# Kernel tuning notes

Measured on AMD Instinct MI355X. Metric: run time of the kernel, lower is better.

Reference implementation:

```python
import jax, jax.numpy as jnp
import numpy as np

IN_SIZE = 1024
OUT_SIZE = 3 * IN_SIZE  # must equal 3*in_size for trigger_a * attn broadcast
B, S = 32, 512


def setup_inputs() -> dict:
    key = jax.random.key(0)
    ks = jax.random.split(key, 8)
    h_state = jax.random.normal(ks[0], (B, S, 2 * IN_SIZE), dtype=jnp.float32)
    x = jax.random.normal(ks[1], (B, S, IN_SIZE), dtype=jnp.float32)
    trigger = jax.random.randint(ks[2], (B,), 0, S)
    mask = jax.random.randint(ks[3], (B, S), 0, 2).astype(jnp.int32)
    # learned params (nn.Linear: y = x @ W.T + b; store pre-transposed as (in, out))
    Wa = jax.random.normal(ks[4], (3 * IN_SIZE, OUT_SIZE), dtype=jnp.float32) / np.sqrt(3 * IN_SIZE)
    ba = jnp.zeros((OUT_SIZE,), dtype=jnp.float32)
    Ws = jax.random.normal(ks[5], (2 * IN_SIZE, OUT_SIZE), dtype=jnp.float32) / np.sqrt(2 * IN_SIZE)
    bs = jnp.zeros((OUT_SIZE,), dtype=jnp.float32)
    return {"h_state": h_state, "x": x, "trigger": trigger, "mask": mask,
            "Wa": Wa, "ba": ba, "Ws": Ws, "bs": bs}


def reference(h_state, x, trigger, mask, Wa, ba, Ws, bs):
    # a: (B, S, 3*in_size)
    a = jnp.concatenate([h_state, x], axis=-1)
    b = a.shape[0]
    # one_hot + masked_select in the original == gather of the trigger row per batch
    trigger_a = a[jnp.arange(b), trigger]  # (B, 3*in_size)
    s = h_state.sum(axis=1)  # (B, 2*in_size)
    # et: (B, S, out_size)
    et = jnp.tanh(a @ Wa + ba + (s @ Ws + bs)[:, None, :])
    # masked_fill where mask == 0 (mask broadcast over feature dim)
    et = jnp.where(mask[:, :, None] == 0, jnp.float32(-1e9), et)
    # softmax over the FEATURE dim (dim=-1), as in the original; dropout in eval mode is identity
    attn = jax.nn.softmax(et, axis=-1)
    # trigger-weighted reduction over the sequence dim
    out = (trigger_a[:, None, :] * attn).sum(axis=1)  # (B, out_size)
    return out
```

## Files before the change

### kernel.cpp

```cpp
#include <hip/hip_runtime.h>
#include <hip/hip_bf16.h>
#include <hip/hip_fp16.h>


namespace {
constexpr int SIN  = 1024;
constexpr int KH   = 2048;
constexpr int NF   = 3072;
constexpr int NBAT = 32;
constexpr int NS   = 512;
constexpr int NM   = NBAT * NS;
constexpr int NDB  = NF / 64;
constexpr int KC   = 8;
constexpr int NKT  = NF / 64;
constexpr int NCH  = 8;
}

typedef unsigned short u16;
typedef __bf16 bf16x8 __attribute__((ext_vector_type(8)));
typedef float  f32x4  __attribute__((ext_vector_type(4)));

#define ASYNC_CP16(gptr, lptr)                                                              \
  __builtin_amdgcn_global_load_lds((__attribute__((address_space(1))) void*)(gptr),         \
                                   (__attribute__((address_space(3))) void*)(lptr), 16, 0, 0)

__device__ __forceinline__ u16 f2b(float f) {
  union { float f; unsigned u; } v; v.f = f;
  unsigned u = v.u;
  u += 0x7FFFu + ((u >> 16) & 1u);
  return (u16)(u >> 16);
}

__global__ __launch_bounds__(64) void k_cnt(const int* __restrict__ mask,
                                            int* __restrict__ bcnt) {
  int b = blockIdx.x, t = threadIdx.x;
  int c = 0;
#pragma unroll
  for (int i = 0; i < NS / 64; ++i) c += mask[b * NS + i * 64 + t];
#pragma unroll
  for (int off = 32; off >= 1; off >>= 1) c += __shfl_down(c, off, 64);
  if (t == 0) bcnt[b] = c;
}

__global__ __launch_bounds__(64) void k_scan(const int* __restrict__ bcnt,
                                             int* __restrict__ boff,
                                             int* __restrict__ meta) {
  if (threadIdx.x == 0) {
    int run = 0;
    for (int b = 0; b < NBAT; ++b) { boff[b] = run; run += bcnt[b]; }
    meta[0] = run;
    meta[1] = (run + 255) & ~255;
  }
}

__global__ __launch_bounds__(512) void k_gather(const int* __restrict__ mask,
                                                const int* __restrict__ boff,
                                                const int* __restrict__ meta,
                                                int* __restrict__ rowmap) {
  __shared__ int ps[NS];
  int b = blockIdx.x, t = threadIdx.x;
  int m = mask[b * NS + t];
  ps[t] = m;
  __syncthreads();
#pragma unroll
  for (int off = 1; off < NS; off <<= 1) {
    int v = (t >= off) ? ps[t - off] : 0;
    __syncthreads();
    ps[t] += v;
    __syncthreads();
  }
  if (m) rowmap[boff[b] + ps[t] - m] = b * NS + t;
  if (b == 0) {
    int Mc = meta[0], McPad = meta[1];
    if (Mc + t < McPad) rowmap[Mc + t] = 0;
  }
}

__global__ __launch_bounds__(256) void k_sum_h(const float* __restrict__ h,
                                               float* __restrict__ s) {
  int b = blockIdx.x;
  int d = blockIdx.y * 256 + threadIdx.x;
  const float* p = h + (size_t)b * NS * KH + d;
  float acc = 0.f;
#pragma unroll 8
  for (int t = 0; t < NS; ++t) acc += p[(size_t)t * KH];
  s[b * KH + d] = acc;
}

__global__ __launch_bounds__(256) void k_base1(const float* __restrict__ s,
                                               const float* __restrict__ Ws,
                                               float* __restrict__ basep) {
  __shared__ float sT[NBAT][KH / KC];
  int f  = blockIdx.x * 256 + threadIdx.x;
  int k0 = blockIdx.y * (KH / KC);
  for (int it = 0; it < NBAT; ++it) {
    int idx = it * 256 + threadIdx.x;
    int b = idx >> 8, kk = idx & 255;
    sT[b][kk] = s[b * KH + k0 + kk];
  }
  __syncthreads();
  float acc[NBAT] = {};
  for (int k = 0; k < KH / KC; ++k) {
    float w = Ws[(size_t)(k0 + k) * NF + f];
#pragma unroll
    for (int b = 0; b < NBAT; ++b) acc[b] += sT[b][k] * w;
  }
#pragma unroll
  for (int b = 0; b < NBAT; ++b)
    basep[((size_t)blockIdx.y * NBAT + b) * NF + f] = acc[b];
}

__global__ __launch_bounds__(256) void k_base2(const float* __restrict__ basep,
                                               const float* __restrict__ ba,
                                               const float* __restrict__ bs,
                                               float* __restrict__ base) {
  int b = blockIdx.x;
  int f = blockIdx.y * 256 + threadIdx.x;
  float acc = 0.f;
#pragma unroll
  for (int kc = 0; kc < KC; ++kc) acc += basep[((size_t)kc * NBAT + b) * NF + f];
  base[b * NF + f] = acc + ba[f] + bs[f];
}

__global__ __launch_bounds__(256) void k_cvt_a(const float* __restrict__ h,
                                               const float* __restrict__ x,
                                               const int* __restrict__ rowmap,
                                               const int* __restrict__ meta,
                                               u16* __restrict__ A) {
  int tid = blockIdx.x * 256 + threadIdx.x;
  int i = tid / (NF / 4);
  if (i >= meta[1]) return;
  int k = (tid - i * (NF / 4)) * 4;
  ushort4 o;
  if (i >= meta[0]) {
    o.x = o.y = o.z = o.w = 0;
  } else {
    int ro = rowmap[i];
    int b = ro >> 9, t = ro & 511;
    const float* src = (k < KH) ? h + ((size_t)b * NS + t) * KH + k
                                : x + ((size_t)b * NS + t) * SIN + (k - KH);
    float4 v = *(const float4*)src;
    o.x = f2b(v.x); o.y = f2b(v.y); o.z = f2b(v.z); o.w = f2b(v.w);
  }
  *(ushort4*)(A + (size_t)i * NF + k) = o;
}

__global__ __launch_bounds__(256) void k_wat(const float* __restrict__ Wa,
                                             u16* __restrict__ WaT) {
  __shared__ float tile[64][65];
  int k0 = blockIdx.x * 64, f0 = blockIdx.y * 64;
  int tid = threadIdx.x;
  int col4 = (tid & 15) * 4, row = tid >> 4;
#pragma unroll
  for (int rr = 0; rr < 64; rr += 16) {
    float4 v = *(const float4*)(Wa + (size_t)(k0 + row + rr) * NF + f0 + col4);
    tile[row + rr][col4 + 0] = v.x; tile[row + rr][col4 + 1] = v.y;
    tile[row + rr][col4 + 2] = v.z; tile[row + rr][col4 + 3] = v.w;
  }
  __syncthreads();
#pragma unroll
  for (int rr = 0; rr < 64; rr += 16) {
    int f = f0 + row + rr;
    ushort4 o;
    o.x = f2b(tile[col4 + 0][row + rr]); o.y = f2b(tile[col4 + 1][row + rr]);
    o.z = f2b(tile[col4 + 2][row + rr]); o.w = f2b(tile[col4 + 3][row + rr]);
    *(ushort4*)(WaT + (size_t)f * NF + k0 + col4) = o;
  }
}

#define LDSOFF(row, gg) ((row) * 32 + ((((gg) ^ (((row) >> 1) & 3))) << 3))

#define LDB4(BUF, KS)                                                        \
  _Pragma("unroll") for (int nf = 0; nf < 4; ++nf) {                         \
    int rb = wc * 64 + nf * 16 + lr;                                         \
    bfr[nf] = *(const bf16x8*)&lds[BUF][1][KS][LDSOFF(rb, g)];               \
  }

#define LDA4(BUF, KS, MH)                                                    \
  _Pragma("unroll") for (int mf = 0; mf < 4; ++mf) {                         \
    int ra = wr * 128 + ((MH) * 4 + mf) * 16 + lr;                           \
    afr[mf] = *(const bf16x8*)&lds[BUF][0][KS][LDSOFF(ra, g)];               \
  }

#define MFMA16(MH)                                                           \
  _Pragma("unroll") for (int mf = 0; mf < 4; ++mf)                           \
  _Pragma("unroll") for (int nf = 0; nf < 4; ++nf)                           \
    acc[(MH) * 4 + mf][nf] = __builtin_amdgcn_mfma_f32_16x16x32_bf16(        \
        afr[mf], bfr[nf], acc[(MH) * 4 + mf][nf], 0, 0, 0);

#define STAGE(SMAT, SBUF, SKS, SKT)                                          \
  if ((SKT) < NKT) {                                                         \
    _Pragma("unroll") for (int q = 0; q < 2; ++q) {                          \
      const u16* src = ((SMAT) ? pB[q] : pA[q]) + (SKT) * 64 + (SKS) * 32;   \
      ASYNC_CP16(src, &lds[SBUF][SMAT][SKS][q * 4096 + wid * 512]);          \
    }                                                                        \
  }

#define PH(BUF, KS, MH, SMAT, SBUF, SKS, SKT)                                \
  {                                                                          \
    if ((MH) == 0) { LDB4(BUF, KS) }                                         \
    LDA4(BUF, KS, MH)                                                        \
    STAGE(SMAT, SBUF, SKS, SKT)                                              \
    __builtin_amdgcn_s_barrier();                                            \
    asm volatile("s_waitcnt lgkmcnt(0)" ::: "memory");                       \
    __builtin_amdgcn_s_setprio(1);                                           \
    MFMA16(MH)                                                               \
    __builtin_amdgcn_s_setprio(0);                                           \
    asm volatile("s_waitcnt vmcnt(6)" ::: "memory");                         \
    __builtin_amdgcn_s_barrier();                                            \
  }

__global__ __launch_bounds__(512, 2) void k_gemm(const u16* __restrict__ A,
                                                 const u16* __restrict__ Wt,
                                                 const float* __restrict__ base,
                                                 const int* __restrict__ rowmap,
                                                 const int* __restrict__ meta,
                                                 __half* __restrict__ P,
                                                 float* __restrict__ Dpart) {
  __shared__ __align__(16) u16 lds[2][2][2][8192];
  const int MT   = meta[1] >> 8;
  const int nact = MT * 12;
  const int flat = blockIdx.x;
  if (flat >= nact) return;
  const int qx = nact >> 3, rx = nact & 7;
  const int xcd = flat & 7, idx = flat >> 3;
  const int swz = (xcd < rx) ? xcd * (qx + 1) + idx
                             : rx * (qx + 1) + (xcd - rx) * qx + idx;
  const int mt = swz / 12, nt = swz - mt * 12;
  const int r0 = mt << 8, c0 = nt << 8;

  const int tid = threadIdx.x;
  const int wid = tid >> 6, lane = tid & 63;
  const int wr = wid >> 2, wc = wid & 3;
  const int g = lane >> 4, lr = lane & 15;

  const u16* pA[2]; const u16* pB[2];
#pragma unroll
  for (int q = 0; q < 2; ++q) {
    int c = q * 512 + tid;
    int row = c >> 2;
    int kc8 = (((c & 3) ^ ((row >> 1) & 3)) << 3);
    pA[q] = A  + (size_t)(r0 + row) * NF + kc8;
    pB[q] = Wt + (size_t)(c0 + row) * NF + kc8;
  }

  f32x4 acc[8][4] = {};
  bf16x8 afr[4], bfr[4];

  STAGE(0, 0, 0, 0) STAGE(1, 0, 0, 0)
  STAGE(0, 0, 1, 0) STAGE(1, 0, 1, 0)
  STAGE(0, 1, 0, 1) STAGE(1, 1, 0, 1)
  asm volatile("s_waitcnt vmcnt(8)" ::: "memory");
  __builtin_amdgcn_s_barrier();

#pragma unroll 1
  for (int i = 0; i < NKT / 2; ++i) {
    const int kt1 = 2 * i + 1, kt2 = 2 * i + 2, kt3 = 2 * i + 3;
    PH(0, 0, 0, 0, 1, 1, kt1)
    PH(0, 0, 1, 1, 1, 1, kt1)
    PH(0, 1, 0, 0, 0, 0, kt2)
    PH(0, 1, 1, 1, 0, 0, kt2)
    PH(1, 0, 0, 0, 0, 1, kt2)
    PH(1, 0, 1, 1, 0, 1, kt2)
    PH(1, 1, 0, 0, 1, 0, kt3)
    PH(1, 1, 1, 1, 1, 0, kt3)
  }

  const int cbase = c0 + wc * 64;
#pragma unroll
  for (int mf = 0; mf < 8; ++mf) {
#pragma unroll
    for (int j = 0; j < 4; ++j) {
      int i = r0 + wr * 128 + mf * 16 + g * 4 + j;
      int b = rowmap[i] >> 9;
      float rs = 0.f;
#pragma unroll
      for (int nf = 0; nf < 4; ++nf) {
        int ccn = cbase + nf * 16 + lr;
        float z  = acc[mf][nf][j] + base[b * NF + ccn];
        z        = fminf(fmaxf(z, -15.f), 15.f);
        float e2 = __expf(2.f * z);
        float th = (e2 - 1.f) / (e2 + 1.f);
        float p  = __expf(th);
        P[(size_t)i * NF + ccn] = __float2half(p);
        rs += p;
      }
#pragma unroll
      for (int off = 1; off < 16; off <<= 1) rs += __shfl_xor(rs, off, 64);
      if (lr == 0) Dpart[(size_t)i * NDB + (cbase >> 6)] = rs;
    }
  }
}

__global__ __launch_bounds__(256) void k_invd(const float* __restrict__ Dpart,
                                              const int* __restrict__ meta,
                                              float* __restrict__ invD) {
  int i = blockIdx.x * 256 + threadIdx.x;
  if (i >= meta[1]) return;
  float d = 0.f;
#pragma unroll
  for (int q = 0; q < NDB; ++q) d += Dpart[(size_t)i * NDB + q];
  invD[i] = 1.0f / d;
}

__global__ __launch_bounds__(256) void k_final1(const __half* __restrict__ P,
                                                const float* __restrict__ invD,
                                                const int* __restrict__ boff,
                                                const int* __restrict__ bcnt,
                                                float* __restrict__ pb) {
  int c = blockIdx.x;
  int b = c >> 3, j = c & 7;
  int f = blockIdx.y * 256 + threadIdx.x;
  int cnt = bcnt[b];
  int lo = j * 64, hi = min(cnt, lo + 64);
  int off = boff[b];
  float acc = 0.f;
  for (int t = lo; t < hi; ++t)
    acc += __half2float(P[(size_t)(off + t) * NF + f]) * invD[off + t];
  pb[(size_t)c * NF + f] = acc;
}

__global__ __launch_bounds__(256) void k_final2(const float* __restrict__ pb,
                                                const int* __restrict__ bcnt,
                                                const float* __restrict__ h,
                                                const float* __restrict__ x,
                                                const int* __restrict__ trig,
                                                float* __restrict__ out) {
  int b = blockIdx.x;
  int f = blockIdx.y * 256 + threadIdx.x;
  float acc = 0.f;
#pragma unroll
  for (int j = 0; j < NCH; ++j) acc += pb[(size_t)(b * NCH + j) * NF + f];
  acc += (float)(NS - bcnt[b]) * (1.0f / (float)NF);
  int tr = trig[b];
  float ta = (f < KH) ? h[((size_t)b * NS + tr) * KH + f]
                      : x[((size_t)b * NS + tr) * SIN + f - KH];
  out[b * NF + f] = acc * ta;
}

extern "C" void kernel_launch(void* const* d_in, const int* in_sizes, int n_in,
                              void* d_out, int out_size, void* d_ws, size_t ws_size,
                              hipStream_t stream) {
  const float* h_state = (const float*)d_in[0];
  const float* x       = (const float*)d_in[1];
  const int*   trigger = (const int*)d_in[2];
  const int*   mask    = (const int*)d_in[3];
  const float* Wa      = (const float*)d_in[4];
  const float* ba      = (const float*)d_in[5];
  const float* Ws      = (const float*)d_in[6];
  const float* bs      = (const float*)d_in[7];
  float*       out     = (float*)d_out;

  char* w = (char*)d_ws;
  u16*    Abf   = (u16*)w;                 w += (size_t)NM * NF * 2;
  u16*    WaT   = (u16*)w;                 w += (size_t)NF * NF * 2;
  __half* P     = (__half*)w;              w += (size_t)NM * NF * 2;
  float*  s     = (float*)w;               w += (size_t)NBAT * KH * 4;
  float*  base  = (float*)w;               w += (size_t)NBAT * NF * 4;
  float*  Dpart = (float*)w;               w += (size_t)NM * NDB * 4;
  float*  basep = (float*)Dpart;
  float*  pb    = (float*)Dpart;
  float*  invD  = (float*)w;               w += (size_t)NM * 4;
  int*    rowmap= (int*)w;                 w += (size_t)NM * 4;
  int*    bcnt  = (int*)w;                 w += 128;
  int*    boff  = (int*)w;                 w += 128;
  int*    meta  = (int*)w;                 w += 128;

  (void)in_sizes; (void)n_in; (void)out_size; (void)ws_size;

  k_cnt   <<<dim3(NBAT), 64, 0, stream>>>(mask, bcnt);
  k_scan  <<<dim3(1), 64, 0, stream>>>(bcnt, boff, meta);
  k_gather<<<dim3(NBAT), 512, 0, stream>>>(mask, boff, meta, rowmap);
  k_sum_h <<<dim3(NBAT, KH / 256), 256, 0, stream>>>(h_state, s);
  k_cvt_a <<<dim3(NM * (NF / 4) / 256), 256, 0, stream>>>(h_state, x, rowmap, meta, Abf);
  k_wat   <<<dim3(NF / 64, NF / 64), 256, 0, stream>>>(Wa, WaT);
  k_base1 <<<dim3(NF / 256, KC), 256, 0, stream>>>(s, Ws, basep);
  k_base2 <<<dim3(NBAT, NF / 256), 256, 0, stream>>>(basep, ba, bs, base);
  k_gemm  <<<dim3((NF / 256) * (NM / 256)), 512, 0, stream>>>(Abf, WaT, base, rowmap, meta, P, Dpart);
  k_invd  <<<dim3(NM / 256), 256, 0, stream>>>(Dpart, meta, invD);
  k_final1<<<dim3(NBAT * NCH, NF / 256), 256, 0, stream>>>(P, invD, boff, bcnt, pb);
  k_final2<<<dim3(NBAT, NF / 256), 256, 0, stream>>>(pb, bcnt, h_state, x, trigger, out);
}
```

Measured before the change: 423.0 us.

## Fuse h-sum with masked bf16 row compaction; merge count/scan; vectorize final1

Merges the mask count and scan kernels into one single-block kernel. Replaces the separate sequence-sum and gather-convert kernels with one kernel that streams h once, accumulating per-chunk partial sums while writing compacted bf16 rows of A. Pad-row zeroing moves into the gather kernel, and the per-chunk partial sums are reduced inside base1. final1 now processes two features per thread with half2 loads and caches invD in shared memory. The fused kernel launches only 256 blocks, each walking 64 rows serially, which may leave much of the GPU idle.

```diff
diff --git a/kernel.cpp b/kernel.cpp
--- a/kernel.cpp
+++ b/kernel.cpp
@@ -31,23 +31,24 @@
   return (u16)(u >> 16);
 }
 
-__global__ __launch_bounds__(64) void k_cnt(const int* __restrict__ mask,
-                                            int* __restrict__ bcnt) {
-  int b = blockIdx.x, t = threadIdx.x;
+__global__ __launch_bounds__(256) void k_prep(const int* __restrict__ mask,
+                                              int* __restrict__ bcnt,
+                                              int* __restrict__ boff,
+                                              int* __restrict__ meta) {
+  int tid = threadIdx.x;
+  int b = tid >> 3, seg = tid & 7;
   int c = 0;
 #pragma unroll
-  for (int i = 0; i < NS / 64; ++i) c += mask[b * NS + i * 64 + t];
-#pragma unroll
-  for (int off = 32; off >= 1; off >>= 1) c += __shfl_down(c, off, 64);
-  if (t == 0) bcnt[b] = c;
-}
-
-__global__ __launch_bounds__(64) void k_scan(const int* __restrict__ bcnt,
-                                             int* __restrict__ boff,
-                                             int* __restrict__ meta) {
-  if (threadIdx.x == 0) {
+  for (int i = 0; i < 64; ++i) c += mask[b * NS + seg * 64 + i];
+  c += __shfl_xor(c, 1, 64);
+  c += __shfl_xor(c, 2, 64);
+  c += __shfl_xor(c, 4, 64);
+  __shared__ int sc[NBAT];
+  if (seg == 0) { sc[b] = c; bcnt[b] = c; }
+  __syncthreads();
+  if (tid == 0) {
     int run = 0;
-    for (int b = 0; b < NBAT; ++b) { boff[b] = run; run += bcnt[b]; }
+    for (int bb = 0; bb < NBAT; ++bb) { boff[bb] = run; run += sc[bb]; }
     meta[0] = run;
     meta[1] = (run + 255) & ~255;
   }
@@ -56,7 +57,8 @@
 __global__ __launch_bounds__(512) void k_gather(const int* __restrict__ mask,
                                                 const int* __restrict__ boff,
                                                 const int* __restrict__ meta,
-                                                int* __restrict__ rowmap) {
+                                                int* __restrict__ rowmap,
+                                                u16* __restrict__ A) {
   __shared__ int ps[NS];
   int b = blockIdx.x, t = threadIdx.x;
   int m = mask[b * NS + t];
@@ -70,33 +72,73 @@
     __syncthreads();
   }
   if (m) rowmap[boff[b] + ps[t] - m] = b * NS + t;
-  if (b == 0) {
-    int Mc = meta[0], McPad = meta[1];
-    if (Mc + t < McPad) rowmap[Mc + t] = 0;
-  }
-}
-
-__global__ __launch_bounds__(256) void k_sum_h(const float* __restrict__ h,
-                                               float* __restrict__ s) {
-  int b = blockIdx.x;
-  int d = blockIdx.y * 256 + threadIdx.x;
-  const float* p = h + (size_t)b * NS * KH + d;
-  float acc = 0.f;
-#pragma unroll 8
-  for (int t = 0; t < NS; ++t) acc += p[(size_t)t * KH];
-  s[b * KH + d] = acc;
-}
-
-__global__ __launch_bounds__(256) void k_base1(const float* __restrict__ s,
+  int Mc = meta[0], pad = meta[1] - Mc;
+  if (b == 0 && t < 256) { if (t < pad) rowmap[Mc + t] = 0; }
+  for (int r = b; r < pad; r += NBAT) {
+    unsigned* row = (unsigned*)(A + (size_t)(Mc + r) * NF);
+    for (int u = t; u < NF / 2; u += 512) row[u] = 0;
+  }
+}
+
+__global__ __launch_bounds__(256) void k_pre(const float* __restrict__ h,
+                                             const float* __restrict__ x,
+                                             const int* __restrict__ mask,
+                                             const int* __restrict__ boff,
+                                             float* __restrict__ spart,
+                                             u16* __restrict__ A) {
+  int b = blockIdx.x, tc = blockIdx.y, tid = threadIdx.x;
+  __shared__ int red[256];
+  __shared__ int ms[64];
+  int pre = 0;
+  for (int u = tid; u < tc * 64; u += 256) pre += mask[b * NS + u];
+  red[tid] = pre;
+  if (tid < 64) ms[tid] = mask[b * NS + tc * 64 + tid];
+  __syncthreads();
+#pragma unroll
+  for (int s2 = 128; s2 > 0; s2 >>= 1) {
+    if (tid < s2) red[tid] += red[tid + s2];
+    __syncthreads();
+  }
+  int idx = boff[b] + red[0];
+  const float* hb = h + ((size_t)b * NS + tc * 64) * KH;
+  const float* xb = x + ((size_t)b * NS + tc * 64) * SIN;
+  float acc[8] = {};
+  for (int t = 0; t < 64; ++t) {
+    float4 v0 = *(const float4*)(hb + (size_t)t * KH + tid * 8);
+    float4 v1 = *(const float4*)(hb + (size_t)t * KH + tid * 8 + 4);
+    acc[0] += v0.x; acc[1] += v0.y; acc[2] += v0.z; acc[3] += v0.w;
+    acc[4] += v1.x; acc[5] += v1.y; acc[6] += v1.z; acc[7] += v1.w;
+    if (ms[t]) {
+      u16* dst = A + (size_t)idx * NF;
+      ushort4 o0; o0.x = f2b(v0.x); o0.y = f2b(v0.y); o0.z = f2b(v0.z); o0.w = f2b(v0.w);
+      ushort4 o1; o1.x = f2b(v1.x); o1.y = f2b(v1.y); o1.z = f2b(v1.z); o1.w = f2b(v1.w);
+      *(ushort4*)(dst + tid * 8)     = o0;
+      *(ushort4*)(dst + tid * 8 + 4) = o1;
+      float4 xv = *(const float4*)(xb + (size_t)t * SIN + tid * 4);
+      ushort4 ox; ox.x = f2b(xv.x); ox.y = f2b(xv.y); ox.z = f2b(xv.z); ox.w = f2b(xv.w);
+      *(ushort4*)(dst + KH + tid * 4) = ox;
+      ++idx;
+    }
+  }
+  float* sp = spart + (size_t)(b * NCH + tc) * KH + tid * 8;
+#pragma unroll
+  for (int j = 0; j < 8; ++j) sp[j] = acc[j];
+}
+
+__global__ __launch_bounds__(256) void k_base1(const float* __restrict__ spart,
                                                const float* __restrict__ Ws,
                                                float* __restrict__ basep) {
   __shared__ float sT[NBAT][KH / KC];
   int f  = blockIdx.x * 256 + threadIdx.x;
   int k0 = blockIdx.y * (KH / KC);
   for (int it = 0; it < NBAT; ++it) {
-    int idx = it * 256 + threadIdx.x;
-    int b = idx >> 8, kk = idx & 255;
-    sT[b][kk] = s[b * KH + k0 + kk];
+    int q = it * 256 + threadIdx.x;
+    int bb = q >> 8, kk = q & 255;
+    float v = 0.f;
+#pragma unroll
+    for (int tc = 0; tc < NCH; ++tc)
+      v += spart[(size_t)(bb * NCH + tc) * KH + k0 + kk];
+    sT[bb][kk] = v;
   }
   __syncthreads();
   float acc[NBAT] = {};
@@ -120,29 +162,6 @@
 #pragma unroll
   for (int kc = 0; kc < KC; ++kc) acc += basep[((size_t)kc * NBAT + b) * NF + f];
   base[b * NF + f] = acc + ba[f] + bs[f];
-}
-
-__global__ __launch_bounds__(256) void k_cvt_a(const float* __restrict__ h,
-                                               const float* __restrict__ x,
-                                               const int* __restrict__ rowmap,
-                                               const int* __restrict__ meta,
-                                               u16* __restrict__ A) {
-  int tid = blockIdx.x * 256 + threadIdx.x;
-  int i = tid / (NF / 4);
-  if (i >= meta[1]) return;
-  int k = (tid - i * (NF / 4)) * 4;
-  ushort4 o;
-  if (i >= meta[0]) {
-    o.x = o.y = o.z = o.w = 0;
-  } else {
-    int ro = rowmap[i];
-    int b = ro >> 9, t = ro & 511;
-    const float* src = (k < KH) ? h + ((size_t)b * NS + t) * KH + k
-                                : x + ((size_t)b * NS + t) * SIN + (k - KH);
-    float4 v = *(const float4*)src;
-    o.x = f2b(v.x); o.y = f2b(v.y); o.z = f2b(v.z); o.w = f2b(v.w);
-  }
-  *(ushort4*)(A + (size_t)i * NF + k) = o;
 }
 
 __global__ __launch_bounds__(256) void k_wat(const float* __restrict__ Wa,
@@ -310,14 +329,23 @@
                                                 float* __restrict__ pb) {
   int c = blockIdx.x;
   int b = c >> 3, j = c & 7;
-  int f = blockIdx.y * 256 + threadIdx.x;
+  int f = blockIdx.y * 512 + threadIdx.x * 2;
   int cnt = bcnt[b];
   int lo = j * 64, hi = min(cnt, lo + 64);
   int off = boff[b];
-  float acc = 0.f;
-  for (int t = lo; t < hi; ++t)
-    acc += __half2float(P[(size_t)(off + t) * NF + f]) * invD[off + t];
-  pb[(size_t)c * NF + f] = acc;
+  __shared__ float ivs[64];
+  if (threadIdx.x < 64 && lo + (int)threadIdx.x < hi)
+    ivs[threadIdx.x] = invD[off + lo + threadIdx.x];
+  __syncthreads();
+  float ax = 0.f, ay = 0.f;
+  for (int t = lo; t < hi; ++t) {
+    __half2 hv = *(const __half2*)(P + (size_t)(off + t) * NF + f);
+    float2 fv = __half22float2(hv);
+    float iv = ivs[t - lo];
+    ax += fv.x * iv; ay += fv.y * iv;
+  }
+  float2 o; o.x = ax; o.y = ay;
+  *(float2*)(pb + (size_t)c * NF + f) = o;
 }
 
 __global__ __launch_bounds__(256) void k_final2(const float* __restrict__ pb,
@@ -355,7 +383,7 @@
   u16*    Abf   = (u16*)w;                 w += (size_t)NM * NF * 2;
   u16*    WaT   = (u16*)w;                 w += (size_t)NF * NF * 2;
   __half* P     = (__half*)w;              w += (size_t)NM * NF * 2;
-  float*  s     = (float*)w;               w += (size_t)NBAT * KH * 4;
+  float*  spart = (float*)w;               w += (size_t)NBAT * NCH * KH * 4;
   float*  base  = (float*)w;               w += (size_t)NBAT * NF * 4;
   float*  Dpart = (float*)w;               w += (size_t)NM * NDB * 4;
   float*  basep = (float*)Dpart;
@@ -368,16 +396,14 @@
 
   (void)in_sizes; (void)n_in; (void)out_size; (void)ws_size;
 
-  k_cnt   <<<dim3(NBAT), 64, 0, stream>>>(mask, bcnt);
-  k_scan  <<<dim3(1), 64, 0, stream>>>(bcnt, boff, meta);
-  k_gather<<<dim3(NBAT), 512, 0, stream>>>(mask, boff, meta, rowmap);
-  k_sum_h <<<dim3(NBAT, KH / 256), 256, 0, stream>>>(h_state, s);
-  k_cvt_a <<<dim3(NM * (NF / 4) / 256), 256, 0, stream>>>(h_state, x, rowmap, meta, Abf);
+  k_prep  <<<dim3(1), 256, 0, stream>>>(mask, bcnt, boff, meta);
+  k_gather<<<dim3(NBAT), 512, 0, stream>>>(mask, boff, meta, rowmap, Abf);
+  k_pre   <<<dim3(NBAT, NCH), 256, 0, stream>>>(h_state, x, mask, boff, spart, Abf);
   k_wat   <<<dim3(NF / 64, NF / 64), 256, 0, stream>>>(Wa, WaT);
-  k_base1 <<<dim3(NF / 256, KC), 256, 0, stream>>>(s, Ws, basep);
+  k_base1 <<<dim3(NF / 256, KC), 256, 0, stream>>>(spart, Ws, basep);
   k_base2 <<<dim3(NBAT, NF / 256), 256, 0, stream>>>(basep, ba, bs, base);
   k_gemm  <<<dim3((NF / 256) * (NM / 256)), 512, 0, stream>>>(Abf, WaT, base, rowmap, meta, P, Dpart);
   k_invd  <<<dim3(NM / 256), 256, 0, stream>>>(Dpart, meta, invD);
-  k_final1<<<dim3(NBAT * NCH, NF / 256), 256, 0, stream>>>(P, invD, boff, bcnt, pb);
+  k_final1<<<dim3(NBAT * NCH, NF / 512), 256, 0, stream>>>(P, invD, boff, bcnt, pb);
   k_final2<<<dim3(NBAT, NF / 256), 256, 0, stream>>>(pb, bcnt, h_state, x, trigger, out);
 }
```

Result: slower. 461.2 us (+9.0%).
